# Kernel optimization log

Measured on AMD Instinct MI355X. Metric: run time of the kernel, lower is better.

## Reference

```python
import jax, jax.numpy as jnp
import numpy as np

RADII = (1.5, 3.0)   # max radii per dilated ring
KS = (32, 64)        # neighbors per ring
OP_C = 64            # per-operator output channels
OUT_C = 256          # agg conv output channels


def setup_inputs() -> dict:
    key = jax.random.key(0)
    k = jax.random.split(key, 8)
    B, N, M, D, C = 4, 8192, 2048, 3, 64
    positions = jax.random.normal(k[0], (B, N, D), dtype=jnp.float32)
    features = jax.random.normal(k[1], (B, N, C), dtype=jnp.float32)
    centers = jax.random.normal(k[2], (B, M, D), dtype=jnp.float32)
    # squared distances in [0, 9) so both rings [1,2.25) and [2.25,9) are hit
    distances = jax.random.uniform(k[3], (B, M, N), dtype=jnp.float32) * 9.0
    W_op0 = jax.random.normal(k[4], (D + C, OP_C), dtype=jnp.float32) * 0.05
    b_op0 = jnp.zeros((OP_C,), dtype=jnp.float32)
    W_op1 = jax.random.normal(k[5], (D + C, OP_C), dtype=jnp.float32) * 0.05
    b_op1 = jnp.zeros((OP_C,), dtype=jnp.float32)
    W_agg = jax.random.normal(k[6], (2 * OP_C, OUT_C), dtype=jnp.float32) * 0.05
    b_agg = jnp.zeros((OUT_C,), dtype=jnp.float32)
    return dict(positions=positions, features=features, centers=centers,
                distances=distances, W_op0=W_op0, b_op0=b_op0,
                W_op1=W_op1, b_op1=b_op1, W_agg=W_agg, b_agg=b_agg)


def reference(positions, features, centers, distances,
              W_op0, b_op0, W_op1, b_op1, W_agg, b_agg):
    B, N, D = positions.shape
    M = centers.shape[1]
    arangeN = jnp.arange(N)
    bidx = jnp.arange(B)[:, None, None]
    min_radius = -1.0  # faithful to source: min_radius**2 == 1 in ring 0
    fs = []
    for max_radius, kk, (W, b) in zip(RADII, KS, ((W_op0, b_op0), (W_op1, b_op1))):
        excluded = (distances >= max_radius ** 2) | (distances < min_radius ** 2)
        idx = jnp.where(excluded, N, arangeN[None, None, :])   # (B,M,N)
        idx = jnp.sort(idx, axis=-1)[:, :, :kk]                # (B,M,k)
        mask = idx != N
        safe = jnp.where(mask, idx, 0)
        pos_g = positions[bidx, safe]                          # (B,M,k,D)
        feat_g = features[bidx, safe]                          # (B,M,k,C)
        rel = pos_g - centers[:, :, None, :]                   # (B,M,k,D)
        h = jax.nn.relu(jnp.concatenate([rel, feat_g], axis=-1) @ W + b)
        h = jnp.where(mask[..., None], h, 0.0)                 # invalid -> zero row
        fs.append(jnp.max(h, axis=2))                          # (B,M,OP_C)
        min_radius = max_radius
    x = jnp.concatenate(fs, axis=-1)                           # (B,M,2*OP_C)
    return jax.nn.relu(x @ W_agg + b_agg)                      # (B,M,OUT_C)
```

## Files before the change

kernel.cpp:

```cpp
#include <hip/hip_runtime.h>
#include <stdint.h>

#define BB 4
#define NN 8192
#define MM 2048
#define CC 64
#define OPC 64
#define OUTC 256
#define K0 32
#define K1 64
#define NCH 12
#define CPW 4

typedef short bf16x8 __attribute__((ext_vector_type(8)));
typedef float f32x4  __attribute__((ext_vector_type(4)));

__device__ __forceinline__ short f2bf(float f) {
    uint32_t u = __float_as_uint(f);
    u += 0x7FFFu + ((u >> 16) & 1u);
    return (short)(u >> 16);
}

template <int ROWS>
__device__ __forceinline__ void stage_row(short (*sA)[ROWS][8], int row,
                                          const float* __restrict__ pos,
                                          const float* __restrict__ feat,
                                          float cx, float cy, float cz) {
    const float4* fp4 = (const float4*)feat;
    float4 q[16];
#pragma unroll
    for (int t = 0; t < 16; ++t) q[t] = fp4[t];
#pragma unroll
    for (int c = 0; c < 8; ++c) {
        float4 a = q[2 * c], b = q[2 * c + 1];
        bf16x8 v;
        v[0] = f2bf(a.x); v[1] = f2bf(a.y); v[2] = f2bf(a.z); v[3] = f2bf(a.w);
        v[4] = f2bf(b.x); v[5] = f2bf(b.y); v[6] = f2bf(b.z); v[7] = f2bf(b.w);
        *(bf16x8*)&sA[c][row][0] = v;
    }
    float rx = pos[0] - cx, ry = pos[1] - cy, rz = pos[2] - cz;
    bf16x8 vr = {f2bf(rx), f2bf(ry), f2bf(rz), 0, 0, 0, 0, 0};
    *(bf16x8*)&sA[8][row][0] = vr;
    bf16x8 z = {0, 0, 0, 0, 0, 0, 0, 0};
    *(bf16x8*)&sA[9][row][0]  = z;
    *(bf16x8*)&sA[10][row][0] = z;
    *(bf16x8*)&sA[11][row][0] = z;
}

__global__ __launch_bounds__(256, 2) void op_kernel(
    const float* __restrict__ positions, const float* __restrict__ features,
    const float* __restrict__ centers,   const float* __restrict__ distances,
    const float* __restrict__ W0, const float* __restrict__ b0,
    const float* __restrict__ W1, const float* __restrict__ b1,
    float* __restrict__ xout)
{
    __shared__ __align__(16) short sA1[4][NCH][K1][8];
    __shared__ __align__(16) short sA0[4][NCH][K0][8];
    __shared__ int s_idx0[4][K0];
    __shared__ int s_idx1[4][K1];

    const int w    = threadIdx.x >> 6;
    const int lane = threadIdx.x & 63;
    const int quad = lane >> 4;
    const int l15  = lane & 15;
    const int gw   = blockIdx.x * 4 + w;

    bf16x8 bfr0[3][4], bfr1[3][4];
#pragma unroll
    for (int kc = 0; kc < 3; ++kc) {
#pragma unroll
        for (int nt = 0; nt < 4; ++nt) {
            const int n = nt * 16 + l15;
            bf16x8 v0, v1;
#pragma unroll
            for (int j = 0; j < 8; ++j) {
                int k = kc * 32 + quad * 8 + j;
                float a0 = 0.f, a1 = 0.f;
                if (k < 64)      { a0 = W0[(3 + k) * OPC + n];  a1 = W1[(3 + k) * OPC + n]; }
                else if (k < 67) { a0 = W0[(k - 64) * OPC + n]; a1 = W1[(k - 64) * OPC + n]; }
                v0[j] = f2bf(a0); v1[j] = f2bf(a1);
            }
            bfr0[kc][nt] = v0; bfr1[kc][nt] = v1;
        }
    }
    float bias0v[4], bias1v[4];
#pragma unroll
    for (int nt = 0; nt < 4; ++nt) {
        bias0v[nt] = b0[nt * 16 + l15];
        bias1v[nt] = b1[nt * 16 + l15];
    }
    const unsigned long long lt = (1ull << lane) - 1ull;

    for (int i = 0; i < CPW; ++i) {
        const int bm = gw * CPW + i;
        const int b  = bm >> 11;

        const float* drow = distances + (size_t)bm * NN;
        int cnt0 = 0, cnt1 = 0;
        for (int base = 0; base < NN; base += 512) {
            if (cnt0 >= K0 && cnt1 >= K1) break;
            float dv[8];
#pragma unroll
            for (int u = 0; u < 8; ++u) dv[u] = drow[base + u * 64 + lane];
#pragma unroll
            for (int u = 0; u < 8; ++u) {
                float d = dv[u];
                bool p0 = (d >= 1.0f)  && (d < 2.25f);
                bool p1 = (d >= 2.25f) && (d < 9.0f);
                unsigned long long m0 = __ballot(p0);
                unsigned long long m1 = __ballot(p1);
                if (cnt0 < K0) {
                    int pos = cnt0 + __popcll(m0 & lt);
                    if (p0 && pos < K0) s_idx0[w][pos] = base + u * 64 + lane;
                    cnt0 += __popcll(m0);
                }
                if (cnt1 < K1) {
                    int pos = cnt1 + __popcll(m1 & lt);
                    if (p1 && pos < K1) s_idx1[w][pos] = base + u * 64 + lane;
                    cnt1 += __popcll(m1);
                }
            }
        }
        cnt0 = min(cnt0, K0);
        cnt1 = min(cnt1, K1);

        const float cx = centers[(size_t)bm * 3 + 0];
        const float cy = centers[(size_t)bm * 3 + 1];
        const float cz = centers[(size_t)bm * 3 + 2];

        {
            int n1 = (lane < cnt1) ? s_idx1[w][lane] : 0;
            stage_row<K1>(sA1[w], lane,
                          positions + (size_t)((size_t)b * NN + n1) * 3,
                          features  + (size_t)((size_t)b * NN + n1) * CC,
                          cx, cy, cz);
        }
        if (lane < K0) {
            int n0 = (lane < cnt0) ? s_idx0[w][lane] : 0;
            stage_row<K0>(sA0[w], lane,
                          positions + (size_t)((size_t)b * NN + n0) * 3,
                          features  + (size_t)((size_t)b * NN + n0) * CC,
                          cx, cy, cz);
        }

        {
            float cm[4] = {0.f, 0.f, 0.f, 0.f};
#pragma unroll
            for (int mt = 0; mt < 4; ++mt) {
                bf16x8 af[3];
#pragma unroll
                for (int kc = 0; kc < 3; ++kc)
                    af[kc] = *(bf16x8*)&sA1[w][kc * 4 + quad][mt * 16 + l15][0];
                f32x4 acc[4];
#pragma unroll
                for (int nt = 0; nt < 4; ++nt)
                    acc[nt] = (f32x4){bias1v[nt], bias1v[nt], bias1v[nt], bias1v[nt]};
#pragma unroll
                for (int kc = 0; kc < 3; ++kc)
#pragma unroll
                    for (int nt = 0; nt < 4; ++nt)
                        acc[nt] = __builtin_amdgcn_mfma_f32_16x16x32_bf16(
                            af[kc], bfr1[kc][nt], acc[nt], 0, 0, 0);
#pragma unroll
                for (int nt = 0; nt < 4; ++nt)
#pragma unroll
                    for (int r = 0; r < 4; ++r) {
                        int m = mt * 16 + quad * 4 + r;
                        float v = (m < cnt1) ? fmaxf(acc[nt][r], 0.f) : 0.f;
                        cm[nt] = fmaxf(cm[nt], v);
                    }
            }
#pragma unroll
            for (int nt = 0; nt < 4; ++nt) {
                cm[nt] = fmaxf(cm[nt], __shfl_xor(cm[nt], 16, 64));
                cm[nt] = fmaxf(cm[nt], __shfl_xor(cm[nt], 32, 64));
            }
            float f = (quad == 0) ? cm[0] : (quad == 1) ? cm[1]
                    : (quad == 2) ? cm[2] : cm[3];
            xout[(size_t)bm * 128 + 64 + lane] = f;
        }

        {
            float cm[4] = {0.f, 0.f, 0.f, 0.f};
#pragma unroll
            for (int mt = 0; mt < 2; ++mt) {
                bf16x8 af[3];
#pragma unroll
                for (int kc = 0; kc < 3; ++kc)
                    af[kc] = *(bf16x8*)&sA0[w][kc * 4 + quad][mt * 16 + l15][0];
                f32x4 acc[4];
#pragma unroll
                for (int nt = 0; nt < 4; ++nt)
                    acc[nt] = (f32x4){bias0v[nt], bias0v[nt], bias0v[nt], bias0v[nt]};
#pragma unroll
                for (int kc = 0; kc < 3; ++kc)
#pragma unroll
                    for (int nt = 0; nt < 4; ++nt)
                        acc[nt] = __builtin_amdgcn_mfma_f32_16x16x32_bf16(
                            af[kc], bfr0[kc][nt], acc[nt], 0, 0, 0);
#pragma unroll
                for (int nt = 0; nt < 4; ++nt)
#pragma unroll
                    for (int r = 0; r < 4; ++r) {
                        int m = mt * 16 + quad * 4 + r;
                        float v = (m < cnt0) ? fmaxf(acc[nt][r], 0.f) : 0.f;
                        cm[nt] = fmaxf(cm[nt], v);
                    }
            }
#pragma unroll
            for (int nt = 0; nt < 4; ++nt) {
                cm[nt] = fmaxf(cm[nt], __shfl_xor(cm[nt], 16, 64));
                cm[nt] = fmaxf(cm[nt], __shfl_xor(cm[nt], 32, 64));
            }
            float f = (quad == 0) ? cm[0] : (quad == 1) ? cm[1]
                    : (quad == 2) ? cm[2] : cm[3];
            xout[(size_t)bm * 128 + lane] = f;
        }
    }
}

__global__ __launch_bounds__(256, 2) void agg_kernel(
    const float* __restrict__ x, const float* __restrict__ Wagg,
    const float* __restrict__ bagg, float* __restrict__ out)
{
    __shared__ float sx[64 * 129];
    const int bm0  = (blockIdx.x >> 1) * 64;
    const int half = blockIdx.x & 1;
    const int t    = threadIdx.x;

#pragma unroll
    for (int q = 0; q < 32; ++q) {
        int f = q * 256 + t;
        int r = f >> 7, c = f & 127;
        sx[r * 129 + c] = x[(size_t)bm0 * 128 + f];
    }
    __syncthreads();

    const int w    = t >> 6;
    const int lane = t & 63;
    const int j0   = half * 128 + w * 32;

    float acc[32];
#pragma unroll
    for (int j = 0; j < 32; ++j) acc[j] = bagg[j0 + j];

#pragma unroll 4
    for (int c = 0; c < 128; ++c) {
        const float xc = sx[lane * 129 + c];
        const float* Wr = Wagg + (size_t)c * OUTC + j0;
#pragma unroll
        for (int j = 0; j < 32; ++j) acc[j] = fmaf(xc, Wr[j], acc[j]);
    }

    float* op = out + (size_t)(bm0 + lane) * OUTC + j0;
#pragma unroll
    for (int j = 0; j < 32; j += 4) {
        float4 v = make_float4(fmaxf(acc[j+0], 0.0f), fmaxf(acc[j+1], 0.0f),
                               fmaxf(acc[j+2], 0.0f), fmaxf(acc[j+3], 0.0f));
        ((float4*)op)[j >> 2] = v;
    }
}

extern "C" void kernel_launch(void* const* d_in, const int* in_sizes, int n_in,
                              void* d_out, int out_size, void* d_ws, size_t ws_size,
                              hipStream_t stream) {
    const float* positions = (const float*)d_in[0];
    const float* features  = (const float*)d_in[1];
    const float* centers   = (const float*)d_in[2];
    const float* distances = (const float*)d_in[3];
    const float* W0        = (const float*)d_in[4];
    const float* b0        = (const float*)d_in[5];
    const float* W1        = (const float*)d_in[6];
    const float* b1        = (const float*)d_in[7];
    const float* Wagg      = (const float*)d_in[8];
    const float* bagg      = (const float*)d_in[9];
    float* out = (float*)d_out;
    float* xws = (float*)d_ws;

    op_kernel<<<512, 256, 0, stream>>>(positions, features, centers, distances,
                                       W0, b0, W1, b1, xws);
    agg_kernel<<<(BB * MM / 64) * 2, 256, 0, stream>>>(xws, Wagg, bagg, out);
}
```

Baseline: 393.6 us.

## Fuse aggregation GEMM into op kernel and trim padded K chunks

The separate agg_kernel is removed. Each wave now keeps its four centers' 128-wide pooled features in shared memory and computes the 256-wide output with ReLU directly, so the workspace round trip and the second launch go away. The padded K dimension is cut from 12 to 9 chunks by having the third MFMA k-step read the single position chunk. Scalar bf16 rounding is replaced with the packed v_cvt_pk_bf16_f32 instruction. In exchange, each wave reads all of Wagg from cache for only four rows, and the agg FMAs now sit at the tail of the op kernel.

```diff
diff --git a/kernel.cpp b/kernel.cpp
--- a/kernel.cpp
+++ b/kernel.cpp
@@ -9,7 +9,7 @@
 #define OUTC 256
 #define K0 32
 #define K1 64
-#define NCH 12
+#define NCH 9
 #define CPW 4
 
 typedef short bf16x8 __attribute__((ext_vector_type(8)));
@@ -19,6 +19,12 @@
     uint32_t u = __float_as_uint(f);
     u += 0x7FFFu + ((u >> 16) & 1u);
     return (short)(u >> 16);
+}
+
+__device__ __forceinline__ uint32_t cvt_pk_bf16(float a, float b) {
+    uint32_t r;
+    asm("v_cvt_pk_bf16_f32 %0, %1, %2" : "=v"(r) : "v"(a), "v"(b));
+    return r;
 }
 
 template <int ROWS>
@@ -33,18 +39,19 @@
 #pragma unroll
     for (int c = 0; c < 8; ++c) {
         float4 a = q[2 * c], b = q[2 * c + 1];
-        bf16x8 v;
-        v[0] = f2bf(a.x); v[1] = f2bf(a.y); v[2] = f2bf(a.z); v[3] = f2bf(a.w);
-        v[4] = f2bf(b.x); v[5] = f2bf(b.y); v[6] = f2bf(b.z); v[7] = f2bf(b.w);
-        *(bf16x8*)&sA[c][row][0] = v;
+        uint4 v;
+        v.x = cvt_pk_bf16(a.x, a.y);
+        v.y = cvt_pk_bf16(a.z, a.w);
+        v.z = cvt_pk_bf16(b.x, b.y);
+        v.w = cvt_pk_bf16(b.z, b.w);
+        *(uint4*)&sA[c][row][0] = v;
     }
     float rx = pos[0] - cx, ry = pos[1] - cy, rz = pos[2] - cz;
-    bf16x8 vr = {f2bf(rx), f2bf(ry), f2bf(rz), 0, 0, 0, 0, 0};
-    *(bf16x8*)&sA[8][row][0] = vr;
-    bf16x8 z = {0, 0, 0, 0, 0, 0, 0, 0};
-    *(bf16x8*)&sA[9][row][0]  = z;
-    *(bf16x8*)&sA[10][row][0] = z;
-    *(bf16x8*)&sA[11][row][0] = z;
+    uint4 vr;
+    vr.x = cvt_pk_bf16(rx, ry);
+    vr.y = cvt_pk_bf16(rz, 0.0f);
+    vr.z = 0u; vr.w = 0u;
+    *(uint4*)&sA[8][row][0] = vr;
 }
 
 __global__ __launch_bounds__(256, 2) void op_kernel(
@@ -52,10 +59,12 @@
     const float* __restrict__ centers,   const float* __restrict__ distances,
     const float* __restrict__ W0, const float* __restrict__ b0,
     const float* __restrict__ W1, const float* __restrict__ b1,
-    float* __restrict__ xout)
+    const float* __restrict__ Wagg, const float* __restrict__ bagg,
+    float* __restrict__ out)
 {
     __shared__ __align__(16) short sA1[4][NCH][K1][8];
     __shared__ __align__(16) short sA0[4][NCH][K0][8];
+    __shared__ float s_x[4][CPW][128];
     __shared__ int s_idx0[4][K0];
     __shared__ int s_idx1[4][K1];
 
@@ -149,8 +158,10 @@
             for (int mt = 0; mt < 4; ++mt) {
                 bf16x8 af[3];
 #pragma unroll
-                for (int kc = 0; kc < 3; ++kc)
-                    af[kc] = *(bf16x8*)&sA1[w][kc * 4 + quad][mt * 16 + l15][0];
+                for (int kc = 0; kc < 3; ++kc) {
+                    int ch = (kc < 2) ? kc * 4 + quad : 8;
+                    af[kc] = *(bf16x8*)&sA1[w][ch][mt * 16 + l15][0];
+                }
                 f32x4 acc[4];
 #pragma unroll
                 for (int nt = 0; nt < 4; ++nt)
@@ -177,7 +188,7 @@
             }
             float f = (quad == 0) ? cm[0] : (quad == 1) ? cm[1]
                     : (quad == 2) ? cm[2] : cm[3];
-            xout[(size_t)bm * 128 + 64 + lane] = f;
+            s_x[w][i][64 + lane] = f;
         }
 
         {
@@ -186,8 +197,10 @@
             for (int mt = 0; mt < 2; ++mt) {
                 bf16x8 af[3];
 #pragma unroll
-                for (int kc = 0; kc < 3; ++kc)
-                    af[kc] = *(bf16x8*)&sA0[w][kc * 4 + quad][mt * 16 + l15][0];
+                for (int kc = 0; kc < 3; ++kc) {
+                    int ch = (kc < 2) ? kc * 4 + quad : 8;
+                    af[kc] = *(bf16x8*)&sA0[w][ch][mt * 16 + l15][0];
+                }
                 f32x4 acc[4];
 #pragma unroll
                 for (int nt = 0; nt < 4; ++nt)
@@ -214,50 +227,44 @@
             }
             float f = (quad == 0) ? cm[0] : (quad == 1) ? cm[1]
                     : (quad == 2) ? cm[2] : cm[3];
-            xout[(size_t)bm * 128 + lane] = f;
-        }
-    }
-}
-
-__global__ __launch_bounds__(256, 2) void agg_kernel(
-    const float* __restrict__ x, const float* __restrict__ Wagg,
-    const float* __restrict__ bagg, float* __restrict__ out)
-{
-    __shared__ float sx[64 * 129];
-    const int bm0  = (blockIdx.x >> 1) * 64;
-    const int half = blockIdx.x & 1;
-    const int t    = threadIdx.x;
-
-#pragma unroll
-    for (int q = 0; q < 32; ++q) {
-        int f = q * 256 + t;
-        int r = f >> 7, c = f & 127;
-        sx[r * 129 + c] = x[(size_t)bm0 * 128 + f];
-    }
-    __syncthreads();
-
-    const int w    = t >> 6;
-    const int lane = t & 63;
-    const int j0   = half * 128 + w * 32;
-
-    float acc[32];
-#pragma unroll
-    for (int j = 0; j < 32; ++j) acc[j] = bagg[j0 + j];
-
-#pragma unroll 4
-    for (int c = 0; c < 128; ++c) {
-        const float xc = sx[lane * 129 + c];
-        const float* Wr = Wagg + (size_t)c * OUTC + j0;
-#pragma unroll
-        for (int j = 0; j < 32; ++j) acc[j] = fmaf(xc, Wr[j], acc[j]);
-    }
-
-    float* op = out + (size_t)(bm0 + lane) * OUTC + j0;
-#pragma unroll
-    for (int j = 0; j < 32; j += 4) {
-        float4 v = make_float4(fmaxf(acc[j+0], 0.0f), fmaxf(acc[j+1], 0.0f),
-                               fmaxf(acc[j+2], 0.0f), fmaxf(acc[j+3], 0.0f));
-        ((float4*)op)[j >> 2] = v;
+            s_x[w][i][lane] = f;
+        }
+    }
+
+    {
+        float4 bias4 = ((const float4*)bagg)[lane];
+        f32x4 acc[CPW];
+#pragma unroll
+        for (int i = 0; i < CPW; ++i)
+            acc[i] = (f32x4){bias4.x, bias4.y, bias4.z, bias4.w};
+
+#pragma unroll 2
+        for (int c4 = 0; c4 < 32; ++c4) {
+            float4 xv[CPW];
+#pragma unroll
+            for (int i = 0; i < CPW; ++i)
+                xv[i] = *(const float4*)&s_x[w][i][c4 * 4];
+#pragma unroll
+            for (int u = 0; u < 4; ++u) {
+                const int c = c4 * 4 + u;
+                float4 wv = *(const float4*)(Wagg + (size_t)c * OUTC + lane * 4);
+#pragma unroll
+                for (int i = 0; i < CPW; ++i) {
+                    const float xc = (u == 0) ? xv[i].x : (u == 1) ? xv[i].y
+                                   : (u == 2) ? xv[i].z : xv[i].w;
+                    acc[i][0] = fmaf(xc, wv.x, acc[i][0]);
+                    acc[i][1] = fmaf(xc, wv.y, acc[i][1]);
+                    acc[i][2] = fmaf(xc, wv.z, acc[i][2]);
+                    acc[i][3] = fmaf(xc, wv.w, acc[i][3]);
+                }
+            }
+        }
+#pragma unroll
+        for (int i = 0; i < CPW; ++i) {
+            float4 o = make_float4(fmaxf(acc[i][0], 0.f), fmaxf(acc[i][1], 0.f),
+                                   fmaxf(acc[i][2], 0.f), fmaxf(acc[i][3], 0.f));
+            *(float4*)(out + (size_t)(gw * CPW + i) * OUTC + lane * 4) = o;
+        }
     }
 }
 
@@ -275,9 +282,8 @@
     const float* Wagg      = (const float*)d_in[8];
     const float* bagg      = (const float*)d_in[9];
     float* out = (float*)d_out;
-    float* xws = (float*)d_ws;
+    (void)d_ws; (void)ws_size;
 
     op_kernel<<<512, 256, 0, stream>>>(positions, features, centers, distances,
-                                       W0, b0, W1, b1, xws);
-    agg_kernel<<<(BB * MM / 64) * 2, 256, 0, stream>>>(xws, Wagg, bagg, out);
-}
+                                       W0, b0, W1, b1, Wagg, bagg, out);
+}
```

Measured after the change: 353.4 us. -10.2%, faster.
